# Kernel optimization log

Measured on AMD Instinct MI355X. Metric: run time of the kernel, lower is better.

Reference implementation:

```python
import jax, jax.numpy as jnp
import numpy as np
from jax import lax

FILTERS = 256
KERNEL = 1
BATCH, T, D = 16, 2048, 512


def conv1d_same(x, w, b):
    # x: [B, T, Cin], w: [K, Cin, Cout], b: [Cout]
    y = lax.conv_general_dilated(
        x, w, window_strides=(1,), padding='SAME',
        dimension_numbers=('NWC', 'WIO', 'NWC'))
    return y + b


def setup_inputs() -> dict:
    key = jax.random.key(0)
    ks = jax.random.split(key, 5)
    inputs = jax.random.normal(ks[0], (BATCH, T, D), dtype=jnp.float32)
    # Glorot-ish init for conv kernels
    W_qkv = jax.random.normal(ks[1], (KERNEL, D, 3 * FILTERS), dtype=jnp.float32) * (1.0 / np.sqrt(D))
    b_qkv = jnp.zeros((3 * FILTERS,), dtype=jnp.float32)
    W_out = jax.random.normal(ks[2], (KERNEL, FILTERS, D), dtype=jnp.float32) * (1.0 / np.sqrt(FILTERS))
    b_out = jnp.zeros((D,), dtype=jnp.float32)
    return {"inputs": inputs, "W_qkv": W_qkv, "b_qkv": b_qkv, "W_out": W_out, "b_out": b_out}


def reference(inputs, W_qkv, b_qkv, W_out, b_out):
    # QKV projection: conv1d(kernel=1) == pointwise linear, kept general via conv
    qkv = conv1d_same(inputs, W_qkv, b_qkv)          # [B, T, 3F]
    q, k, v = jnp.split(qkv, 3, axis=-1)             # each [B, T, F]
    scale = jnp.sqrt(jnp.asarray(FILTERS, dtype=q.dtype))
    score = jnp.einsum('btf,bsf->bts', q, k) / scale  # [B, T, T]
    attn = jax.nn.softmax(score, axis=-1)
    context = jnp.einsum('bts,bsf->btf', attn, v)    # [B, T, F]
    output = conv1d_same(context, W_out, b_out)      # [B, T, D]
    return inputs + output
```

## Files before the change

### kernel.cpp

```cpp
#include <hip/hip_runtime.h>

typedef __bf16 bf16_t;
typedef __attribute__((ext_vector_type(8))) __bf16 bf16x8;
typedef __attribute__((ext_vector_type(4))) __bf16 bf16x4;
typedef __attribute__((ext_vector_type(4))) float f32x4;

#define GLL16(gsrc, ldst)                                                                   \
  __builtin_amdgcn_global_load_lds(                                                         \
      (const __attribute__((address_space(1))) unsigned int*)(gsrc),                        \
      (__attribute__((address_space(3))) unsigned int*)(ldst), 16, 0, 0)

#define BATCH 16
#define TT    2048
#define DD    512
#define FF    256
#define MTOT  (BATCH * TT)

__global__ __launch_bounds__(256) void cast_x_kernel(const float* __restrict__ x,
                                                     bf16_t* __restrict__ xb, int n4) {
  int stride = gridDim.x * blockDim.x;
  for (int i = blockIdx.x * blockDim.x + threadIdx.x; i < n4; i += stride) {
    float4 v = ((const float4*)x)[i];
    bf16x4 o;
    o[0] = (bf16_t)v.x; o[1] = (bf16_t)v.y; o[2] = (bf16_t)v.z; o[3] = (bf16_t)v.w;
    ((bf16x4*)xb)[i] = o;
  }
}

__global__ __launch_bounds__(256) void cast_w_kernel(const float* __restrict__ Wqkv,
                                                     const float* __restrict__ Wout,
                                                     bf16_t* __restrict__ WqkvT,
                                                     bf16_t* __restrict__ WoutT) {
  int t = blockIdx.x * blockDim.x + threadIdx.x;
  if (t < 768 * 512) {
    int n = t >> 9, k = t & 511;
    WqkvT[t] = (bf16_t)Wqkv[k * 768 + n];
  } else {
    int t2 = t - 768 * 512;
    if (t2 < 512 * 256) {
      int n = t2 >> 8, k = t2 & 255;
      WoutT[t2] = (bf16_t)Wout[k * 512 + n];
    }
  }
}

__global__ __launch_bounds__(256) void gemm_qkv_kernel(const bf16_t* __restrict__ A,
                                                       const bf16_t* __restrict__ Bt,
                                                       const float* __restrict__ bias,
                                                       bf16_t* __restrict__ Qo,
                                                       bf16_t* __restrict__ Ko,
                                                       bf16_t* __restrict__ Vt) {
  __shared__ __align__(16) bf16_t Al[2][128 * 32];
  __shared__ __align__(16) bf16_t Bl[2][128 * 32];
  const int tid = threadIdx.x;
  const int l = tid & 63, w = tid >> 6;
  const int g = l >> 4, r = l & 15;
  const int wm = w >> 1, wn = w & 1;
  const int lin = blockIdx.x;
  const int wid = (lin & 7) * 192 + (lin >> 3);
  const int m0 = (wid / 6) * 128;
  const int n0 = (wid % 6) * 128;
  const int lda = 512, ldb = 512;
  const bf16_t* Abase = A + (size_t)m0 * lda;
  const bf16_t* Bbase = Bt + (size_t)n0 * ldb;

  f32x4 acc[4][4] = {};

  auto stage = [&](int kt, int bufi) {
    const int k0 = kt * 32;
#pragma unroll
    for (int rnd = 0; rnd < 2; ++rnd) {
      int idx = rnd * 256 + tid;
      int row = idx >> 2, d = idx & 3;
      int sc = d ^ ((row >> 1) & 3);
      GLL16(Abase + row * lda + k0 + sc * 8, &Al[bufi][idx * 8]);
    }
#pragma unroll
    for (int rnd = 0; rnd < 2; ++rnd) {
      int idx = rnd * 256 + tid;
      int row = idx >> 2, d = idx & 3;
      int sc = d ^ ((row >> 1) & 3);
      GLL16(Bbase + row * ldb + k0 + sc * 8, &Bl[bufi][idx * 8]);
    }
  };

  stage(0, 0);
  __syncthreads();
  int buf = 0;
  const int NK = 512 / 32;
  for (int kt = 0; kt < NK; ++kt) {
    if (kt + 1 < NK) stage(kt + 1, buf ^ 1);
    bf16x8 af[4], bfr[4];
#pragma unroll
    for (int mi = 0; mi < 4; ++mi) {
      int row = wm * 64 + mi * 16 + r;
      int cc = g ^ ((row >> 1) & 3);
      af[mi] = *(const bf16x8*)&Al[buf][row * 32 + cc * 8];
    }
#pragma unroll
    for (int ni = 0; ni < 4; ++ni) {
      int row = wn * 64 + ni * 16 + r;
      int cc = g ^ ((row >> 1) & 3);
      bfr[ni] = *(const bf16x8*)&Bl[buf][row * 32 + cc * 8];
    }
#pragma unroll
    for (int mi = 0; mi < 4; ++mi)
#pragma unroll
      for (int ni = 0; ni < 4; ++ni)
        acc[mi][ni] = __builtin_amdgcn_mfma_f32_16x16x32_bf16(af[mi], bfr[ni], acc[mi][ni], 0, 0, 0);
    __syncthreads();
    buf ^= 1;
  }

  const int qsel = n0 >> 8;
#pragma unroll
  for (int mi = 0; mi < 4; ++mi) {
    int row0 = m0 + wm * 64 + mi * 16 + g * 4;
#pragma unroll
    for (int ni = 0; ni < 4; ++ni) {
      int col = n0 + wn * 64 + ni * 16 + r;
      float bv = bias[col];
      int cl = col & 255;
      if (qsel == 2) {
        bf16x4 pk;
#pragma unroll
        for (int i = 0; i < 4; ++i) pk[i] = (bf16_t)(acc[mi][ni][i] + bv);
        int b = row0 >> 11, t0 = row0 & 2047;
        *(bf16x4*)&Vt[((size_t)(b * 256 + cl)) * 2048 + t0] = pk;
      } else {
        bf16_t* dst = (qsel == 0) ? Qo : Ko;
#pragma unroll
        for (int i = 0; i < 4; ++i)
          dst[(size_t)(row0 + i) * 256 + cl] = (bf16_t)(acc[mi][ni][i] + bv);
      }
    }
  }
}

__global__ __launch_bounds__(512, 2) void attn_kernel(const bf16_t* __restrict__ Q,
                                                      const bf16_t* __restrict__ K,
                                                      const bf16_t* __restrict__ Vt,
                                                      bf16_t* __restrict__ ctx) {
  __shared__ __align__(16) bf16_t Kl[2][64 * 256];
  __shared__ __align__(16) bf16_t Vl[2][256 * 64];
  __shared__ __align__(16) bf16_t Pl[8][16 * 64];
  const int tid = threadIdx.x;
  const int l = tid & 63, w = tid >> 6;
  const int g = l >> 4, r = l & 15;
  const int lin = blockIdx.x;
  const int wid = (lin & 7) * 32 + (lin >> 3);
  const int b = wid >> 4;
  const int q0 = (wid & 15) * 128 + w * 16;
  const bf16_t* Kb = K + ((size_t)b * TT) * 256;
  const bf16_t* Vb = Vt + (size_t)b * 256 * TT;

  bf16x8 qf[8];
  const bf16_t* Qrow = Q + ((size_t)(b * TT) + q0 + r) * 256;
#pragma unroll
  for (int kf = 0; kf < 8; ++kf) qf[kf] = *(const bf16x8*)(Qrow + kf * 32 + g * 8);

  f32x4 cacc[16] = {};
  float m_run = -3.0e38f, l_run = 0.0f;

  auto stage = [&](int kv0, int bi) {
#pragma unroll
    for (int rnd = 0; rnd < 4; ++rnd) {
      int idx = rnd * 512 + tid;
      int row = idx >> 5, d = idx & 31;
      int sc = d ^ (row & 7);
      GLL16(Kb + (size_t)(kv0 + row) * 256 + sc * 8, &Kl[bi][idx * 8]);
    }
#pragma unroll
    for (int rnd = 0; rnd < 4; ++rnd) {
      int idx = rnd * 512 + tid;
      int row = idx >> 3, d = idx & 7;
      int sc = d ^ (row & 7);
      GLL16(Vb + (size_t)row * TT + kv0 + sc * 8, &Vl[bi][idx * 8]);
    }
  };

  stage(0, 0);
  __syncthreads();
  int buf = 0;

  for (int kv0 = 0; kv0 < TT; kv0 += 64) {
    if (kv0 + 64 < TT) stage(kv0 + 64, buf ^ 1);

    f32x4 st[4] = {};
#pragma unroll
    for (int kf = 0; kf < 8; ++kf) {
#pragma unroll
      for (int kvf = 0; kvf < 4; ++kvf) {
        int row = kvf * 16 + r;
        int c = kf * 4 + g;
        bf16x8 kfr = *(const bf16x8*)&Kl[buf][row * 256 + ((c ^ (row & 7)) * 8)];
        st[kvf] = __builtin_amdgcn_mfma_f32_16x16x32_bf16(kfr, qf[kf], st[kvf], 0, 0, 0);
      }
    }

    float tmax = -3.0e38f;
    float s[4][4];
#pragma unroll
    for (int kvf = 0; kvf < 4; ++kvf)
#pragma unroll
      for (int i = 0; i < 4; ++i) {
        s[kvf][i] = st[kvf][i] * 0.0625f;
        tmax = fmaxf(tmax, s[kvf][i]);
      }
    tmax = fmaxf(tmax, __shfl_xor(tmax, 16));
    tmax = fmaxf(tmax, __shfl_xor(tmax, 32));
    if (!__all(tmax - m_run <= 8.0f)) {
      float mnew = fmaxf(m_run, tmax);
      float alpha = __expf(m_run - mnew);
      l_run *= alpha;
#pragma unroll
      for (int fc = 0; fc < 16; ++fc)
#pragma unroll
        for (int i = 0; i < 4; ++i) cacc[fc][i] *= alpha;
      m_run = mnew;
    }
    float psum = 0.0f;
#pragma unroll
    for (int kvf = 0; kvf < 4; ++kvf) {
      bf16x4 pk;
#pragma unroll
      for (int i = 0; i < 4; ++i) {
        float p = __expf(s[kvf][i] - m_run);
        psum += p;
        pk[i] = (bf16_t)p;
      }
      int widx = r * 64 + ((((kvf * 2 + (g >> 1)) ^ (r & 7)) << 3) | ((g & 1) * 4));
      *(bf16x4*)&Pl[w][widx] = pk;
    }
    psum += __shfl_xor(psum, 16);
    psum += __shfl_xor(psum, 32);
    l_run += psum;

#pragma unroll
    for (int kk = 0; kk < 2; ++kk) {
      bf16x8 pf = *(const bf16x8*)&Pl[w][r * 64 + (((kk * 4 + g) ^ (r & 7)) << 3)];
#pragma unroll
      for (int fc = 0; fc < 16; ++fc) {
        int row = fc * 16 + r;
        int c = kk * 4 + g;
        bf16x8 vf = *(const bf16x8*)&Vl[buf][row * 64 + ((c ^ (row & 7)) * 8)];
        cacc[fc] = __builtin_amdgcn_mfma_f32_16x16x32_bf16(vf, pf, cacc[fc], 0, 0, 0);
      }
    }

    __syncthreads();
    buf ^= 1;
  }

  float inv = 1.0f / l_run;
  bf16_t* crow = ctx + ((size_t)(b * TT) + q0 + r) * 256;
#pragma unroll
  for (int fc = 0; fc < 16; ++fc) {
    bf16x4 pk;
#pragma unroll
    for (int i = 0; i < 4; ++i) pk[i] = (bf16_t)(cacc[fc][i] * inv);
    *(bf16x4*)(crow + fc * 16 + g * 4) = pk;
  }
}

__global__ __launch_bounds__(256) void gemm_out_kernel(const bf16_t* __restrict__ A,
                                                       const bf16_t* __restrict__ Bt,
                                                       const float* __restrict__ bias,
                                                       const float* __restrict__ X,
                                                       float* __restrict__ Out) {
  __shared__ __align__(16) bf16_t Al[2][128 * 32];
  __shared__ __align__(16) bf16_t Bl[2][128 * 32];
  const int tid = threadIdx.x;
  const int l = tid & 63, w = tid >> 6;
  const int g = l >> 4, r = l & 15;
  const int wm = w >> 1, wn = w & 1;
  const int lin = blockIdx.x;
  const int wid = (lin & 7) * 128 + (lin >> 3);
  const int m0 = (wid >> 2) * 128;
  const int n0 = (wid & 3) * 128;
  const int lda = 256, ldb = 256;
  const bf16_t* Abase = A + (size_t)m0 * lda;
  const bf16_t* Bbase = Bt + (size_t)n0 * ldb;

  f32x4 acc[4][4] = {};

  auto stage = [&](int kt, int bufi) {
    const int k0 = kt * 32;
#pragma unroll
    for (int rnd = 0; rnd < 2; ++rnd) {
      int idx = rnd * 256 + tid;
      int row = idx >> 2, d = idx & 3;
      int sc = d ^ ((row >> 1) & 3);
      GLL16(Abase + row * lda + k0 + sc * 8, &Al[bufi][idx * 8]);
    }
#pragma unroll
    for (int rnd = 0; rnd < 2; ++rnd) {
      int idx = rnd * 256 + tid;
      int row = idx >> 2, d = idx & 3;
      int sc = d ^ ((row >> 1) & 3);
      GLL16(Bbase + row * ldb + k0 + sc * 8, &Bl[bufi][idx * 8]);
    }
  };

  stage(0, 0);
  __syncthreads();
  int buf = 0;
  const int NK = 256 / 32;
  for (int kt = 0; kt < NK; ++kt) {
    if (kt + 1 < NK) stage(kt + 1, buf ^ 1);
    bf16x8 af[4], bfr[4];
#pragma unroll
    for (int mi = 0; mi < 4; ++mi) {
      int row = wm * 64 + mi * 16 + r;
      int cc = g ^ ((row >> 1) & 3);
      af[mi] = *(const bf16x8*)&Al[buf][row * 32 + cc * 8];
    }
#pragma unroll
    for (int ni = 0; ni < 4; ++ni) {
      int row = wn * 64 + ni * 16 + r;
      int cc = g ^ ((row >> 1) & 3);
      bfr[ni] = *(const bf16x8*)&Bl[buf][row * 32 + cc * 8];
    }
#pragma unroll
    for (int mi = 0; mi < 4; ++mi)
#pragma unroll
      for (int ni = 0; ni < 4; ++ni)
        acc[mi][ni] = __builtin_amdgcn_mfma_f32_16x16x32_bf16(af[mi], bfr[ni], acc[mi][ni], 0, 0, 0);
    __syncthreads();
    buf ^= 1;
  }

#pragma unroll
  for (int mi = 0; mi < 4; ++mi) {
    int row0 = m0 + wm * 64 + mi * 16 + g * 4;
#pragma unroll
    for (int ni = 0; ni < 4; ++ni) {
      int col = n0 + wn * 64 + ni * 16 + r;
      float bv = bias[col];
#pragma unroll
      for (int i = 0; i < 4; ++i) {
        size_t off = (size_t)(row0 + i) * 512 + col;
        Out[off] = acc[mi][ni][i] + bv + X[off];
      }
    }
  }
}

extern "C" void kernel_launch(void* const* d_in, const int* in_sizes, int n_in,
                              void* d_out, int out_size, void* d_ws, size_t ws_size,
                              hipStream_t stream) {
  const float* X    = (const float*)d_in[0];
  const float* Wqkv = (const float*)d_in[1];
  const float* bqkv = (const float*)d_in[2];
  const float* Wout = (const float*)d_in[3];
  const float* bout = (const float*)d_in[4];
  float* out = (float*)d_out;

  char* ws = (char*)d_ws;
  bf16_t* Xbf   = (bf16_t*)ws;
  bf16_t* ctx   = Xbf;
  bf16_t* WqkvT = (bf16_t*)(ws + 33554432);
  bf16_t* WoutT = (bf16_t*)(ws + 34340864);
  bf16_t* Qb    = (bf16_t*)(ws + 34603008);
  bf16_t* Kb    = (bf16_t*)(ws + 51380224);
  bf16_t* Vt    = (bf16_t*)(ws + 68157440);

  cast_x_kernel<<<2048, 256, 0, stream>>>(X, Xbf, (MTOT * DD) / 4);
  cast_w_kernel<<<2048, 256, 0, stream>>>(Wqkv, Wout, WqkvT, WoutT);
  gemm_qkv_kernel<<<1536, 256, 0, stream>>>(Xbf, WqkvT, bqkv, Qb, Kb, Vt);
  attn_kernel<<<256, 512, 0, stream>>>(Qb, Kb, Vt, ctx);
  gemm_out_kernel<<<1024, 256, 0, stream>>>(ctx, WoutT, bout, X, out);
}
```

Baseline: 315.6 us.

## Shrink attention tiles to 64 queries and 32 keys; merge cast kernels

The attention kernel now runs 4 waves of 16 query rows per block (64 queries) over 512 blocks, with KV tiles of 32 instead of 64. This halves LDS use per block, which may allow more blocks per CU and spreads the work over more CUs. The V tile drops its XOR swizzle. s_setprio is raised around the MFMA sections to favour matrix issue. The two cast kernels are merged into one launch to save launch overhead. In exchange, each block reloads K/V for fewer queries, so global traffic and the number of loop iterations and barriers roughly double.

```diff
diff --git a/kernel.cpp b/kernel.cpp
--- a/kernel.cpp
+++ b/kernel.cpp
@@ -16,30 +16,29 @@
 #define FF    256
 #define MTOT  (BATCH * TT)
 
-__global__ __launch_bounds__(256) void cast_x_kernel(const float* __restrict__ x,
-                                                     bf16_t* __restrict__ xb, int n4) {
-  int stride = gridDim.x * blockDim.x;
-  for (int i = blockIdx.x * blockDim.x + threadIdx.x; i < n4; i += stride) {
+__global__ __launch_bounds__(256) void cast_all_kernel(const float* __restrict__ x,
+                                                       bf16_t* __restrict__ xb,
+                                                       const float* __restrict__ Wqkv,
+                                                       const float* __restrict__ Wout,
+                                                       bf16_t* __restrict__ WqkvT,
+                                                       bf16_t* __restrict__ WoutT) {
+  const int t0 = blockIdx.x * blockDim.x + threadIdx.x;
+  const int stride = gridDim.x * blockDim.x;
+  const int n4 = (MTOT * DD) / 4;
+  for (int i = t0; i < n4; i += stride) {
     float4 v = ((const float4*)x)[i];
     bf16x4 o;
     o[0] = (bf16_t)v.x; o[1] = (bf16_t)v.y; o[2] = (bf16_t)v.z; o[3] = (bf16_t)v.w;
     ((bf16x4*)xb)[i] = o;
   }
-}
-
-__global__ __launch_bounds__(256) void cast_w_kernel(const float* __restrict__ Wqkv,
-                                                     const float* __restrict__ Wout,
-                                                     bf16_t* __restrict__ WqkvT,
-                                                     bf16_t* __restrict__ WoutT) {
-  int t = blockIdx.x * blockDim.x + threadIdx.x;
-  if (t < 768 * 512) {
-    int n = t >> 9, k = t & 511;
-    WqkvT[t] = (bf16_t)Wqkv[k * 768 + n];
-  } else {
-    int t2 = t - 768 * 512;
-    if (t2 < 512 * 256) {
-      int n = t2 >> 8, k = t2 & 255;
-      WoutT[t2] = (bf16_t)Wout[k * 512 + n];
+  for (int i = t0; i < 768 * 512 + 512 * 256; i += stride) {
+    if (i < 768 * 512) {
+      int n = i >> 9, k = i & 511;
+      WqkvT[i] = (bf16_t)Wqkv[k * 768 + n];
+    } else {
+      int i2 = i - 768 * 512;
+      int n = i2 >> 8, k = i2 & 255;
+      WoutT[i2] = (bf16_t)Wout[k * 512 + n];
     }
   }
 }
@@ -137,20 +136,20 @@
   }
 }
 
-__global__ __launch_bounds__(512, 2) void attn_kernel(const bf16_t* __restrict__ Q,
+__global__ __launch_bounds__(256, 2) void attn_kernel(const bf16_t* __restrict__ Q,
                                                       const bf16_t* __restrict__ K,
                                                       const bf16_t* __restrict__ Vt,
                                                       bf16_t* __restrict__ ctx) {
-  __shared__ __align__(16) bf16_t Kl[2][64 * 256];
-  __shared__ __align__(16) bf16_t Vl[2][256 * 64];
-  __shared__ __align__(16) bf16_t Pl[8][16 * 64];
+  __shared__ __align__(16) bf16_t Kl[2][32 * 256];
+  __shared__ __align__(16) bf16_t Vl[2][256 * 32];
+  __shared__ __align__(16) bf16_t Pl[4][16 * 32];
   const int tid = threadIdx.x;
   const int l = tid & 63, w = tid >> 6;
   const int g = l >> 4, r = l & 15;
   const int lin = blockIdx.x;
-  const int wid = (lin & 7) * 32 + (lin >> 3);
-  const int b = wid >> 4;
-  const int q0 = (wid & 15) * 128 + w * 16;
+  const int wid = (lin & 7) * 64 + (lin >> 3);
+  const int b = wid >> 5;
+  const int q0 = (wid & 31) * 64 + w * 16;
   const bf16_t* Kb = K + ((size_t)b * TT) * 256;
   const bf16_t* Vb = Vt + (size_t)b * 256 * TT;
 
@@ -165,17 +164,16 @@
   auto stage = [&](int kv0, int bi) {
 #pragma unroll
     for (int rnd = 0; rnd < 4; ++rnd) {
-      int idx = rnd * 512 + tid;
+      int idx = rnd * 256 + tid;
       int row = idx >> 5, d = idx & 31;
       int sc = d ^ (row & 7);
       GLL16(Kb + (size_t)(kv0 + row) * 256 + sc * 8, &Kl[bi][idx * 8]);
     }
 #pragma unroll
     for (int rnd = 0; rnd < 4; ++rnd) {
-      int idx = rnd * 512 + tid;
-      int row = idx >> 3, d = idx & 7;
-      int sc = d ^ (row & 7);
-      GLL16(Vb + (size_t)row * TT + kv0 + sc * 8, &Vl[bi][idx * 8]);
+      int idx = rnd * 256 + tid;
+      int row = idx >> 2, d = idx & 3;
+      GLL16(Vb + (size_t)row * TT + kv0 + d * 8, &Vl[bi][idx * 8]);
     }
   };
 
@@ -183,25 +181,27 @@
   __syncthreads();
   int buf = 0;
 
-  for (int kv0 = 0; kv0 < TT; kv0 += 64) {
-    if (kv0 + 64 < TT) stage(kv0 + 64, buf ^ 1);
-
-    f32x4 st[4] = {};
+  for (int kv0 = 0; kv0 < TT; kv0 += 32) {
+    if (kv0 + 32 < TT) stage(kv0 + 32, buf ^ 1);
+
+    f32x4 st[2] = {};
+    __builtin_amdgcn_s_setprio(1);
 #pragma unroll
     for (int kf = 0; kf < 8; ++kf) {
 #pragma unroll
-      for (int kvf = 0; kvf < 4; ++kvf) {
+      for (int kvf = 0; kvf < 2; ++kvf) {
         int row = kvf * 16 + r;
-        int c = kf * 4 + g;
-        bf16x8 kfr = *(const bf16x8*)&Kl[buf][row * 256 + ((c ^ (row & 7)) * 8)];
+        int chunk = (kf * 4 + g) ^ (r & 7);
+        bf16x8 kfr = *(const bf16x8*)&Kl[buf][row * 256 + chunk * 8];
         st[kvf] = __builtin_amdgcn_mfma_f32_16x16x32_bf16(kfr, qf[kf], st[kvf], 0, 0, 0);
       }
     }
-
+    __builtin_amdgcn_s_setprio(0);
+
+    float s[2][4];
     float tmax = -3.0e38f;
-    float s[4][4];
-#pragma unroll
-    for (int kvf = 0; kvf < 4; ++kvf)
+#pragma unroll
+    for (int kvf = 0; kvf < 2; ++kvf)
 #pragma unroll
       for (int i = 0; i < 4; ++i) {
         s[kvf][i] = st[kvf][i] * 0.0625f;
@@ -221,7 +221,7 @@
     }
     float psum = 0.0f;
 #pragma unroll
-    for (int kvf = 0; kvf < 4; ++kvf) {
+    for (int kvf = 0; kvf < 2; ++kvf) {
       bf16x4 pk;
 #pragma unroll
       for (int i = 0; i < 4; ++i) {
@@ -229,24 +229,22 @@
         psum += p;
         pk[i] = (bf16_t)p;
       }
-      int widx = r * 64 + ((((kvf * 2 + (g >> 1)) ^ (r & 7)) << 3) | ((g & 1) * 4));
-      *(bf16x4*)&Pl[w][widx] = pk;
+      int eidx = r * 32 + (((kvf * 2 + (g >> 1)) ^ (r & 3)) << 3) + (g & 1) * 4;
+      *(bf16x4*)&Pl[w][eidx] = pk;
     }
     psum += __shfl_xor(psum, 16);
     psum += __shfl_xor(psum, 32);
     l_run += psum;
 
-#pragma unroll
-    for (int kk = 0; kk < 2; ++kk) {
-      bf16x8 pf = *(const bf16x8*)&Pl[w][r * 64 + (((kk * 4 + g) ^ (r & 7)) << 3)];
-#pragma unroll
-      for (int fc = 0; fc < 16; ++fc) {
-        int row = fc * 16 + r;
-        int c = kk * 4 + g;
-        bf16x8 vf = *(const bf16x8*)&Vl[buf][row * 64 + ((c ^ (row & 7)) * 8)];
-        cacc[fc] = __builtin_amdgcn_mfma_f32_16x16x32_bf16(vf, pf, cacc[fc], 0, 0, 0);
-      }
-    }
+    bf16x8 pf = *(const bf16x8*)&Pl[w][r * 32 + ((g ^ (r & 3)) << 3)];
+    __builtin_amdgcn_s_setprio(1);
+#pragma unroll
+    for (int fc = 0; fc < 16; ++fc) {
+      int row = fc * 16 + r;
+      bf16x8 vf = *(const bf16x8*)&Vl[buf][row * 32 + g * 8];
+      cacc[fc] = __builtin_amdgcn_mfma_f32_16x16x32_bf16(vf, pf, cacc[fc], 0, 0, 0);
+    }
+    __builtin_amdgcn_s_setprio(0);
 
     __syncthreads();
     buf ^= 1;
@@ -365,9 +363,8 @@
   bf16_t* Kb    = (bf16_t*)(ws + 51380224);
   bf16_t* Vt    = (bf16_t*)(ws + 68157440);
 
-  cast_x_kernel<<<2048, 256, 0, stream>>>(X, Xbf, (MTOT * DD) / 4);
-  cast_w_kernel<<<2048, 256, 0, stream>>>(Wqkv, Wout, WqkvT, WoutT);
+  cast_all_kernel<<<2048, 256, 0, stream>>>(X, Xbf, Wqkv, Wout, WqkvT, WoutT);
   gemm_qkv_kernel<<<1536, 256, 0, stream>>>(Xbf, WqkvT, bqkv, Qb, Kb, Vt);
-  attn_kernel<<<256, 512, 0, stream>>>(Qb, Kb, Vt, ctx);
+  attn_kernel<<<512, 256, 0, stream>>>(Qb, Kb, Vt, ctx);
   gemm_out_kernel<<<1024, 256, 0, stream>>>(ctx, WoutT, bout, X, out);
 }
```

Result: slower. 328.2 us (+4.0%).
